# Kernel optimization log

Measured on AMD Instinct MI355X. Metric: run time of the kernel, lower is better.

The kernel has to match this reference:

```python
import jax, jax.numpy as jnp
import numpy as np
import math

B, S, D, H = 16, 1024, 1024, 16
HD = D // H                      # 64 head dim
MLP_H = int(int(D * 4.0) * 2 / 3)  # 2730 SwiGLU hidden
EPS = 1e-6


def _rmsnorm(h, w):
    # fp32 RMSNorm over last dim
    v = jnp.mean(h * h, axis=-1, keepdims=True)
    return w * (h * jax.lax.rsqrt(v + EPS))


def _rope(x):
    # x: [B, H, S, HD]; standard rotary, half-split convention
    hd = x.shape[-1]
    pos = jnp.arange(x.shape[-2], dtype=jnp.float32)
    inv = 1.0 / (10000.0 ** (jnp.arange(0, hd, 2, dtype=jnp.float32) / hd))
    fr = pos[:, None] * inv[None, :]          # [S, HD/2]
    cos, sin = jnp.cos(fr), jnp.sin(fr)
    x1, x2 = jnp.split(x, 2, axis=-1)
    return jnp.concatenate([x1 * cos - x2 * sin, x1 * sin + x2 * cos], axis=-1)


def setup_inputs() -> dict:
    key = jax.random.key(0)
    ks = jax.random.split(key, 16)
    sc = 0.02
    return {
        "x": jax.random.normal(ks[0], (B, S, D), jnp.float32),
        "c": jax.random.normal(ks[1], (B, D), jnp.float32),
        "w_qkv": jax.random.normal(ks[2], (D, 3 * D), jnp.float32) * sc,
        "b_qkv": jnp.zeros((3 * D,), jnp.float32),
        "w_proj": jax.random.normal(ks[3], (D, D), jnp.float32) * sc,
        "b_proj": jnp.zeros((D,), jnp.float32),
        "w12": jax.random.normal(ks[4], (D, 2 * MLP_H), jnp.float32) * sc,
        "b12": jnp.zeros((2 * MLP_H,), jnp.float32),
        "w3": jax.random.normal(ks[5], (MLP_H, D), jnp.float32) * sc,
        "b3": jnp.zeros((D,), jnp.float32),
        "w_ada": jax.random.normal(ks[6], (D, 6 * D), jnp.float32) * sc,
        "b_ada": jnp.zeros((6 * D,), jnp.float32),
        "norm1_w": jnp.ones((D,), jnp.float32),
        "norm2_w": jnp.ones((D,), jnp.float32),
        "qn_w": jnp.ones((HD,), jnp.float32),
        "kn_w": jnp.ones((HD,), jnp.float32),
    }


def _forward(x, c, w_qkv, b_qkv, w_proj, b_proj, w12, b12, w3, b3,
             w_ada, b_ada, norm1_w, norm2_w, qn_w, kn_w):
    # adaLN modulation params
    ada = jax.nn.silu(c) @ w_ada + b_ada               # [B, 6D]
    sh_a, sc_a, g_a, sh_m, sc_m, g_m = jnp.split(ada, 6, axis=-1)

    def modulate(h, shift, scale):
        return h * (1.0 + scale[:, None, :]) + shift[:, None, :]

    # --- attention branch ---
    h = modulate(_rmsnorm(x, norm1_w), sh_a, sc_a)     # [B, S, D]
    qkv = (h @ w_qkv + b_qkv).reshape(B, S, 3, H, HD)
    qkv = jnp.transpose(qkv, (2, 0, 3, 1, 4))          # [3, B, H, S, HD]
    q, k, v = qkv[0], qkv[1], qkv[2]
    q = _rope(_rmsnorm(q, qn_w))
    k = _rope(_rmsnorm(k, kn_w))
    scores = jnp.einsum('bhqd,bhkd->bhqk', q, k) / math.sqrt(HD)
    attn = jax.nn.softmax(scores, axis=-1)
    o = jnp.einsum('bhqk,bhkd->bhqd', attn, v)         # [B, H, S, HD]
    o = jnp.transpose(o, (0, 2, 1, 3)).reshape(B, S, D)
    o = o @ w_proj + b_proj
    x = x + g_a[:, None, :] * o

    # --- SwiGLU MLP branch ---
    h = modulate(_rmsnorm(x, norm2_w), sh_m, sc_m)
    x12 = h @ w12 + b12
    x1, x2 = jnp.split(x12, 2, axis=-1)
    mlp = (jax.nn.silu(x1) * x2) @ w3 + b3
    return x + g_m[:, None, :] * mlp


def reference(x, c, w_qkv, b_qkv, w_proj, b_proj, w12, b12, w3, b3,
              w_ada, b_ada, norm1_w, norm2_w, qn_w, kn_w):
    return _forward(x, c, w_qkv, b_qkv, w_proj, b_proj, w12, b12, w3, b3,
                    w_ada, b_ada, norm1_w, norm2_w, qn_w, kn_w)
```

## Files before the change

### kernel.cpp

```cpp
#include <hip/hip_runtime.h>
#include <hip/hip_bf16.h>
#include <math.h>

namespace {

constexpr int Bb = 16;
constexpr int Ss = 1024;
constexpr int Dd = 1024;
constexpr int Hh = 16;
constexpr int HD = 64;
constexpr int MLPH = 2730;
constexpr int MLPH_PAD = 2752;
constexpr int ADA_LD = 6144;
constexpr int NR = Bb * Ss;

typedef __attribute__((ext_vector_type(8))) short bf16x8;
typedef __attribute__((ext_vector_type(4))) float f32x4;
typedef __hip_bfloat16 bf16;
typedef unsigned int u32;

__device__ __forceinline__ float bf2f(bf16 v){ return __bfloat162float(v); }
__device__ __forceinline__ bf16 f2bf(float v){ return __float2bfloat16(v); }
__device__ __forceinline__ short f2bfs(float v){ bf16 t = __float2bfloat16(v); return __builtin_bit_cast(short, t); }

__device__ __forceinline__ f32x4 mfma16(bf16x8 a, bf16x8 b, f32x4 c){
  return __builtin_amdgcn_mfma_f32_16x16x32_bf16(a, b, c, 0, 0, 0);
}

__device__ __forceinline__ void gload16(const void* g, void* l){
  __builtin_amdgcn_global_load_lds(
      (const __attribute__((address_space(1))) u32*)g,
      (__attribute__((address_space(3))) u32*)l, 16, 0, 0);
}


__global__ void k_silu(const float* __restrict__ c, float* __restrict__ out, int n){
  int i = blockIdx.x*256 + threadIdx.x;
  if(i < n){ float v = c[i]; out[i] = v / (1.f + __expf(-v)); }
}

__global__ __launch_bounds__(256) void k_ada(const float* __restrict__ sc,
    const float* __restrict__ w, const float* __restrict__ bias, float* __restrict__ ada){
  __shared__ float red[4][Bb][64];
  int tid = threadIdx.x;
  int jj = tid & 63, ks = tid >> 6;
  int j = blockIdx.x*64 + jj;
  float acc[Bb];
  #pragma unroll
  for(int b=0;b<Bb;++b) acc[b] = 0.f;
  for(int k=ks*256; k<ks*256+256; ++k){
    float wv = w[(size_t)k*ADA_LD + j];
    #pragma unroll
    for(int b=0;b<Bb;++b) acc[b] += sc[b*Dd + k] * wv;
  }
  #pragma unroll
  for(int b=0;b<Bb;++b) red[ks][b][jj] = acc[b];
  __syncthreads();
  #pragma unroll
  for(int rep=0;rep<4;++rep){
    int idx = rep*256 + tid;
    int b = idx >> 6, j2 = idx & 63;
    float s = red[0][b][j2]+red[1][b][j2]+red[2][b][j2]+red[3][b][j2];
    ada[(size_t)b*ADA_LD + blockIdx.x*64 + j2] = s + bias[blockIdx.x*64 + j2];
  }
}

__global__ void k_rope_tab(float2* __restrict__ tab){
  int i = blockIdx.x*256 + threadIdx.x;
  int s = i >> 5, f = i & 31;
  float inv = powf(10000.f, -((float)(2*f)) / 64.f);
  float fr = (float)s * inv;
  float sv, cv;
  sincosf(fr, &sv, &cv);
  tab[i] = make_float2(cv, sv);
}

__global__ void k_transpose(const float* __restrict__ in, bf16* __restrict__ out,
                            int R, int C, int Rpad){
  __shared__ short tile[32][33];
  int tx = threadIdx.x & 31, ty = threadIdx.x >> 5;
  int tr0 = blockIdx.x*32, tc0 = blockIdx.y*32;
  #pragma unroll
  for(int i=0;i<4;++i){
    int r = tr0 + ty + i*8, cc = tc0 + tx;
    short v = 0;
    if(r < R && cc < C) v = f2bfs(in[(size_t)r*C + cc]);
    tile[ty+i*8][tx] = v;
  }
  __syncthreads();
  #pragma unroll
  for(int i=0;i<4;++i){
    int oc = tc0 + ty + i*8;
    int orow = tr0 + tx;
    if(oc < C && orow < Rpad)
      out[(size_t)oc*Rpad + orow] = __builtin_bit_cast(bf16, tile[tx][ty+i*8]);
  }
}

__global__ __launch_bounds__(256) void k_norm_mod(const float* __restrict__ x,
    const float* __restrict__ w, const float* __restrict__ shift, const float* __restrict__ scale,
    bf16* __restrict__ out){
  int r = blockIdx.x;
  int b = r >> 10;
  int t = threadIdx.x;
  const float* xr = x + (size_t)r*Dd;
  float v[4]; float ss = 0.f;
  #pragma unroll
  for(int i=0;i<4;++i){
    float f = xr[t*4+i];
    v[i] = f; ss += f*f;
  }
  #pragma unroll
  for(int m=1;m<64;m<<=1) ss += __shfl_xor(ss, m);
  __shared__ float red[4];
  if((t & 63) == 0) red[t>>6] = ss;
  __syncthreads();
  float tot = red[0]+red[1]+red[2]+red[3];
  float rms = rsqrtf(tot * (1.f/Dd) + 1e-6f);
  #pragma unroll
  for(int i=0;i<4;++i){
    int ccol = t*4+i;
    float h = v[i]*rms*w[ccol];
    float scv = scale[(size_t)b*ADA_LD + ccol];
    float shv = shift[(size_t)b*ADA_LD + ccol];
    out[(size_t)r*Dd + ccol] = f2bf(h*(1.f+scv) + shv);
  }
}

__global__ __launch_bounds__(256) void k_qknorm(bf16* __restrict__ qkv,
    const float* __restrict__ qw, const float* __restrict__ kw,
    const float2* __restrict__ tab){
  int bs = blockIdx.x;
  int s = bs & (Ss-1);
  int tid = threadIdx.x;
  int wv = tid >> 6, lane = tid & 63;
  int isK = wv >> 1;
  int chunk = (wv & 1)*64 + lane;
  int c = chunk & 7;
  int h = chunk >> 3;
  int dih = c*8;
  bf16* p = qkv + (size_t)bs*3072 + isK*Dd + h*HD + dih;
  bf16x8 v = *(const bf16x8*)p;
  float x[8]; float ss = 0.f;
  #pragma unroll
  for(int i=0;i<8;++i){ x[i] = bf2f(__builtin_bit_cast(bf16,(short)v[i])); ss += x[i]*x[i]; }
  ss += __shfl_xor(ss,1); ss += __shfl_xor(ss,2); ss += __shfl_xor(ss,4);
  float rms = rsqrtf(ss*(1.f/HD) + 1e-6f);
  const float* wn = isK ? kw : qw;
  float xn[8];
  #pragma unroll
  for(int i=0;i<8;++i) xn[i] = x[i]*rms*wn[dih+i];
  u32 pk[4], pq[4];
  #pragma unroll
  for(int i=0;i<4;++i)
    pk[i] = (u32)(unsigned short)f2bfs(xn[2*i]) |
            ((u32)(unsigned short)f2bfs(xn[2*i+1]) << 16);
  #pragma unroll
  for(int i=0;i<4;++i) pq[i] = __shfl_xor((int)pk[i], 4);
  float px[8];
  #pragma unroll
  for(int i=0;i<4;++i){
    px[2*i]   = bf2f(__builtin_bit_cast(bf16,(short)(pq[i] & 0xffff)));
    px[2*i+1] = bf2f(__builtin_bit_cast(bf16,(short)(pq[i] >> 16)));
  }
  const float2* tb = tab + s*32 + (c & 3)*8;
  float qs = isK ? 1.f : 0.18033688f;
  bf16x8 o;
  #pragma unroll
  for(int i=0;i<8;++i){
    float2 cs = tb[i];
    float r = (c < 4) ? (xn[i]*cs.x - px[i]*cs.y) : (px[i]*cs.y + xn[i]*cs.x);
    o[i] = f2bfs(r*qs);
  }
  *(bf16x8*)p = o;
}

template<int MODE>
__global__ __launch_bounds__(256, 2) void k_gemm(
    const bf16* __restrict__ A, int lda,
    const bf16* __restrict__ BT, long long b2off, int ldb,
    const float* __restrict__ bias1, const float* __restrict__ bias2,
    int K,
    const float* __restrict__ res, const float* __restrict__ gate,
    void* __restrict__ outp, int ldo)
{
  constexpr int BN  = (MODE==3) ? 64 : 128;
  constexpr int NFR = (MODE==3) ? 2  : 4;
  alignas(16) __shared__ short As[2][128*32];
  alignas(16) __shared__ short Bs[2][BN*32];
  alignas(16) __shared__ short Bs2[(MODE==3)?2:1][(MODE==3)?BN*32:8];

  int tid = threadIdx.x;
  int lane = tid & 63, wid = tid >> 6;
  int wm = wid >> 1, wn = wid & 1;
  int l15 = lane & 15, l4 = lane >> 4;
  int brow = blockIdx.x * 128;
  int bcol = blockIdx.y * BN;

  int r0 = tid >> 2, s0 = tid & 3;
  int r1 = r0 + 64;
  int k80 = s0 ^ ((r0 >> 1) & 3);
  int k81 = s0 ^ ((r1 >> 1) & 3);

  const bf16* a0 = A  + (size_t)(brow+r0)*lda + k80*8;
  const bf16* a1 = A  + (size_t)(brow+r1)*lda + k81*8;
  const bf16* b0 = BT + (size_t)(bcol+r0)*ldb + k80*8;
  const bf16* b1 = BT + (size_t)(bcol+r1)*ldb + k81*8;

  f32x4 zero4 = {0.f,0.f,0.f,0.f};
  f32x4 acc[4][NFR], acc2[4][NFR];
  #pragma unroll
  for(int m=0;m<4;++m)
    #pragma unroll
    for(int n=0;n<NFR;++n){ acc[m][n]=zero4; acc2[m][n]=zero4; }

  auto STAGE = [&](int kt, int buf){
    int ko = kt << 5;
    gload16(a0 + ko, &As[buf][tid*8]);
    gload16(a1 + ko, &As[buf][(tid+256)*8]);
    gload16(b0 + ko, &Bs[buf][tid*8]);
    if constexpr (MODE!=3) gload16(b1 + ko, &Bs[buf][(tid+256)*8]);
    if constexpr (MODE==3) gload16(b0 + b2off + ko, &Bs2[buf][tid*8]);
  };

  const int nk = K >> 5;
  STAGE(0, 0);
  __syncthreads();

  int cur = 0;
  for(int kt=0; kt<nk; ++kt){
    if(kt+1 < nk) STAGE(kt+1, cur^1);

    bf16x8 af[4], bfr[NFR], bfr2[NFR];
    #pragma unroll
    for(int m=0;m<4;++m){
      int rr = wm*64 + m*16 + l15;
      int sl = l4 ^ ((rr >> 1) & 3);
      af[m] = *(const bf16x8*)&As[cur][rr*32 + sl*8];
    }
    #pragma unroll
    for(int n=0;n<NFR;++n){
      int rr = wn*(16*NFR) + n*16 + l15;
      int sl = l4 ^ ((rr >> 1) & 3);
      bfr[n] = *(const bf16x8*)&Bs[cur][rr*32 + sl*8];
      if constexpr (MODE==3)
        bfr2[n] = *(const bf16x8*)&Bs2[cur][rr*32 + sl*8];
    }
    #pragma unroll
    for(int m=0;m<4;++m){
      #pragma unroll
      for(int n=0;n<NFR;++n){
        acc[m][n] = mfma16(af[m], bfr[n], acc[m][n]);
        if constexpr (MODE==3) acc2[m][n] = mfma16(af[m], bfr2[n], acc2[m][n]);
      }
    }
    __syncthreads();
    cur ^= 1;
  }

  #pragma unroll
  for(int m=0;m<4;++m){
    #pragma unroll
    for(int n=0;n<NFR;++n){
      #pragma unroll
      for(int j=0;j<4;++j){
        int r  = brow + wm*64 + m*16 + l4*4 + j;
        int cc = bcol + wn*(16*NFR) + n*16 + l15;
        float v = acc[m][n][j];
        if constexpr (MODE==0){
          v += bias1[cc];
          ((bf16*)outp)[(size_t)r*ldo + cc] = f2bf(v);
        } else if constexpr (MODE==1){
          v += bias1[cc];
          int b = r >> 10;
          float xr = res[(size_t)r*Dd + cc];
          ((float*)outp)[(size_t)r*ldo + cc] = xr + gate[(size_t)b*ADA_LD + cc]*v;
        } else {
          float o = 0.f;
          if(cc < MLPH){
            float v1 = v + bias1[cc];
            float v2 = acc2[m][n][j] + bias2[cc];
            o = (v1/(1.f+__expf(-v1)))*v2;
          }
          ((bf16*)outp)[(size_t)r*ldo + cc] = f2bf(o);
        }
      }
    }
  }
}

__global__ __launch_bounds__(256) void k_attn(const bf16* __restrict__ qkv, bf16* __restrict__ obuf){
  alignas(16) __shared__ short Ks[64*64];
  alignas(16) __shared__ short VTs[64*64];
  alignas(16) __shared__ short Ps[128*64];

  int flatb = blockIdx.x;
  int low3 = flatb & 7;
  int rest = flatb >> 3;
  int qb   = rest & 7;
  int bh   = ((rest >> 3) << 3) | low3;
  int b = bh >> 4, h = bh & 15;

  int tid = threadIdx.x;
  int lane = tid & 63, w = tid >> 6;
  int l15 = lane & 15, l4 = lane >> 4;

  const bf16* base = qkv + (size_t)b*Ss*3072 + h*HD;

  bf16x8 aq[2][2];
  #pragma unroll
  for(int hi=0;hi<2;++hi)
    #pragma unroll
    for(int hf=0;hf<2;++hf)
      aq[hi][hf] = *(const bf16x8*)(base +
          (size_t)(qb*128 + w*32 + hi*16 + l15)*3072 + hf*32 + l4*8);

  int r0 = tid >> 3, c0 = tid & 7;
  int khcol = (c0 ^ (r0 & 7)) * 8;
  bf16x8 kreg[2], vreg[2];
  #pragma unroll
  for(int ch=0; ch<2; ++ch){
    int rr = r0 + ch*32;
    kreg[ch] = *(const bf16x8*)(base + Dd   + (size_t)rr*3072 + khcol);
    vreg[ch] = *(const bf16x8*)(base + 2*Dd + (size_t)rr*3072 + c0*8);
  }

  f32x4 zero4 = {0.f,0.f,0.f,0.f};
  f32x4 acc_o[2][4];
  float mrow[2], lrow[2];
  #pragma unroll
  for(int hi=0;hi<2;++hi){
    mrow[hi] = -1e30f; lrow[hi] = 0.f;
    #pragma unroll
    for(int an=0;an<4;++an) acc_o[hi][an] = zero4;
  }

  const float THR = 11.54f;

  for(int kb=0; kb<Ss/64; ++kb){
    if(kb) __syncthreads();
    #pragma unroll
    for(int ch=0; ch<2; ++ch){
      *(bf16x8*)&Ks[(tid + ch*256)*8] = kreg[ch];
      int vr = r0 + ch*32;
      #pragma unroll
      for(int i=0;i<8;++i){
        int g = i ^ c0;
        VTs[(c0*8 + i)*64 + (vr ^ (g<<3))] = vreg[ch][i];
      }
    }
    if(kb+1 < Ss/64){
      #pragma unroll
      for(int ch=0; ch<2; ++ch){
        int rr = (kb+1)*64 + r0 + ch*32;
        kreg[ch] = *(const bf16x8*)(base + Dd   + (size_t)rr*3072 + khcol);
        vreg[ch] = *(const bf16x8*)(base + 2*Dd + (size_t)rr*3072 + c0*8);
      }
    }
    __syncthreads();

    #pragma unroll
    for(int hi=0; hi<2; ++hi){
      f32x4 sacc[4];
      #pragma unroll
      for(int an=0;an<4;++an) sacc[an]=zero4;
      __builtin_amdgcn_s_setprio(1);
      #pragma unroll
      for(int an=0;an<4;++an){
        int R = an*16 + l15;
        bf16x8 bk0 = *(const bf16x8*)&Ks[R*64 + ((l4     ^ (R&7)))*8];
        bf16x8 bk1 = *(const bf16x8*)&Ks[R*64 + (((4|l4) ^ (R&7)))*8];
        sacc[an] = mfma16(bk0, aq[hi][0], sacc[an]);
        sacc[an] = mfma16(bk1, aq[hi][1], sacc[an]);
      }
      __builtin_amdgcn_s_setprio(0);

      float mx = -1e30f;
      #pragma unroll
      for(int an=0;an<4;++an)
        #pragma unroll
        for(int j=0;j<4;++j) mx = fmaxf(mx, sacc[an][j]);
      mx = fmaxf(mx, __shfl_xor(mx, 16));
      mx = fmaxf(mx, __shfl_xor(mx, 32));
      bool grow = mx > mrow[hi] + THR;
      if(__any(grow)){
        float mnew = fmaxf(mrow[hi], mx);
        float corr = exp2f(mrow[hi] - mnew);
        mrow[hi] = mnew;
        lrow[hi] *= corr;
        float cj[4];
        #pragma unroll
        for(int j=0;j<4;++j) cj[j] = __shfl(corr, l4*4 + j);
        #pragma unroll
        for(int an=0;an<4;++an)
          #pragma unroll
          for(int j=0;j<4;++j) acc_o[hi][an][j] *= cj[j];
      }
      float psum = 0.f;
      #pragma unroll
      for(int an=0;an<4;++an)
        #pragma unroll
        for(int j=0;j<4;++j){
          float pv = exp2f(sacc[an][j] - mrow[hi]);
          sacc[an][j] = pv; psum += pv;
        }
      psum += __shfl_xor(psum, 16);
      psum += __shfl_xor(psum, 32);
      lrow[hi] += psum;

      int prow = w*32 + hi*16 + l15;
      int pg = (l15 & 7) << 3;
      #pragma unroll
      for(int an=0;an<4;++an)
        #pragma unroll
        for(int j=0;j<4;++j)
          Ps[prow*64 + ((an*16 + l4*4 + j) ^ pg)] = f2bfs(sacc[an][j]);
      bf16x8 pa0 = *(const bf16x8*)&Ps[prow*64 + ((l4*8)      ^ pg)];
      bf16x8 pa1 = *(const bf16x8*)&Ps[prow*64 + ((32 + l4*8) ^ pg)];
      __builtin_amdgcn_s_setprio(1);
      #pragma unroll
      for(int an2=0;an2<4;++an2){
        int dR = an2*16 + l15;
        int g = ((dR & 7) ^ ((dR >> 3) & 7)) << 3;
        bf16x8 bv0 = *(const bf16x8*)&VTs[dR*64 + ((l4*8)      ^ g)];
        bf16x8 bv1 = *(const bf16x8*)&VTs[dR*64 + ((32 + l4*8) ^ g)];
        acc_o[hi][an2] = mfma16(pa0, bv0, acc_o[hi][an2]);
        acc_o[hi][an2] = mfma16(pa1, bv1, acc_o[hi][an2]);
      }
      __builtin_amdgcn_s_setprio(0);
    }
  }
  #pragma unroll
  for(int hi=0;hi<2;++hi){
    float lr[4];
    #pragma unroll
    for(int j=0;j<4;++j) lr[j] = __shfl(lrow[hi], l4*4 + j);
    #pragma unroll
    for(int an2=0;an2<4;++an2)
      #pragma unroll
      for(int j=0;j<4;++j){
        int r = qb*128 + w*32 + hi*16 + l4*4 + j;
        float ov = acc_o[hi][an2][j] / lr[j];
        obuf[((size_t)b*Ss + r)*Dd + h*HD + an2*16 + l15] = f2bf(ov);
      }
  }
}

}

extern "C" void kernel_launch(void* const* d_in, const int* in_sizes, int n_in,
                              void* d_out, int out_size, void* d_ws, size_t ws_size,
                              hipStream_t stream){
  const float* x      = (const float*)d_in[0];
  const float* c      = (const float*)d_in[1];
  const float* w_qkv  = (const float*)d_in[2];
  const float* b_qkv  = (const float*)d_in[3];
  const float* w_proj = (const float*)d_in[4];
  const float* b_proj = (const float*)d_in[5];
  const float* w12    = (const float*)d_in[6];
  const float* b12    = (const float*)d_in[7];
  const float* w3     = (const float*)d_in[8];
  const float* b3     = (const float*)d_in[9];
  const float* w_ada  = (const float*)d_in[10];
  const float* b_ada  = (const float*)d_in[11];
  const float* n1w    = (const float*)d_in[12];
  const float* n2w    = (const float*)d_in[13];
  const float* qnw    = (const float*)d_in[14];
  const float* knw    = (const float*)d_in[15];
  float* out = (float*)d_out;
  (void)in_sizes; (void)n_in; (void)out_size;

  constexpr size_t WS_NEED = 227254272ull;
  if (ws_size < WS_NEED) return;

  char* ws = (char*)d_ws;
  float*  silu_c = (float*)(ws + 0);
  float*  ada    = (float*)(ws + 65536);
  float2* ropet  = (float2*)(ws + 458752);
  bf16*   wqkvT  = (bf16*)(ws + 720896);
  bf16*   wprojT = (bf16*)(ws + 7012352);
  bf16*   w12T   = (bf16*)(ws + 9109504);
  bf16*   w3T    = (bf16*)(ws + 20291584);
  bf16*   hbuf   = (bf16*)(ws + 25927680);
  bf16*   qkvb   = (bf16*)(ws + 59482112);
  float*  xmid   = (float*)(ws + 160145408);
  bf16*   obuf   = hbuf;
  bf16*   h2     = hbuf;
  bf16*   mlpmid = qkvb;

  k_silu<<<64,256,0,stream>>>(c, silu_c, Bb*Dd);
  k_rope_tab<<<128,256,0,stream>>>(ropet);
  k_ada<<<96,256,0,stream>>>(silu_c, w_ada, b_ada, ada);
  k_transpose<<<dim3(32,96),256,0,stream>>>(w_qkv, wqkvT, 1024, 3072, 1024);
  k_transpose<<<dim3(32,32),256,0,stream>>>(w_proj, wprojT, 1024, 1024, 1024);
  k_transpose<<<dim3(32,171),256,0,stream>>>(w12, w12T, 1024, 5460, 1024);
  k_transpose<<<dim3(86,32),256,0,stream>>>(w3, w3T, 2730, 1024, 2752);

  k_norm_mod<<<NR,256,0,stream>>>(x, n1w, ada + 0, ada + 1024, hbuf);
  k_gemm<0><<<dim3(128,24),256,0,stream>>>(hbuf,1024, wqkvT,0,1024,
      b_qkv,nullptr, 1024, nullptr,nullptr, qkvb,3072);
  k_qknorm<<<NR,256,0,stream>>>(qkvb, qnw, knw, ropet);
  k_attn<<<2048,256,0,stream>>>(qkvb, obuf);
  k_gemm<1><<<dim3(128,8),256,0,stream>>>(obuf,1024, wprojT,0,1024,
      b_proj,nullptr, 1024, x, ada + 2048, xmid,1024);

  k_norm_mod<<<NR,256,0,stream>>>(xmid, n2w, ada + 3072, ada + 4096, h2);
  k_gemm<3><<<dim3(128,43),256,0,stream>>>(h2,1024, w12T,(long long)MLPH*1024,1024,
      b12, b12 + MLPH, 1024, nullptr,nullptr, mlpmid, MLPH_PAD);
  k_gemm<1><<<dim3(128,8),256,0,stream>>>(mlpmid,MLPH_PAD, w3T,0,MLPH_PAD,
      b3,nullptr, MLPH_PAD, xmid, ada + 5120, out,1024);
}
```

Measured before the change: 937.7 us.

## Add 256x256 eight-wave pipelined GEMM for QKV, proj and down GEMMs

Adds a new GEMM kernel with 512 threads and 256x256 output tiles, K-steps of 64, and separate A and B half-tile LDS buffers. Loads for the next steps are interleaved with four MFMA phases, using explicit barriers, waitcnt and setprio. It is used for the QKV, attention-projection and MLP down-projection GEMMs. The SwiGLU up-projection keeps the old kernel as a specialised k_gemm3. The goal is more data reuse per tile and better overlap of global loads with MFMA. The cost is about 128KB of LDS per block, which likely allows only one block per CU, and hand-written wait counts that could be fragile.

```diff
diff --git a/kernel.cpp b/kernel.cpp
--- a/kernel.cpp
+++ b/kernel.cpp
@@ -175,27 +175,135 @@
   *(bf16x8*)p = o;
 }
 
+#define LDA8(M,KH) (*(const bf16x8*)&Ah[((M)*16 + l15)*64 + ((((KH)*4 + l4) ^ l7))*8])
+#define PHASE8(M0, STAGE_STMT, GATE_STMT) do{ \
+  bf16x8 a0k0 = LDA8(M0,0), a0k1 = LDA8(M0,1), a1k0 = LDA8(M0+1,0), a1k1 = LDA8(M0+1,1); \
+  STAGE_STMT; \
+  __builtin_amdgcn_s_barrier(); \
+  asm volatile("s_waitcnt lgkmcnt(0)" ::: "memory"); \
+  __builtin_amdgcn_sched_barrier(0); \
+  __builtin_amdgcn_s_setprio(1); \
+  acc[M0][0]=mfma16(a0k0,bfrag[0][0],acc[M0][0]); acc[M0][0]=mfma16(a0k1,bfrag[0][1],acc[M0][0]); \
+  acc[M0][1]=mfma16(a0k0,bfrag[1][0],acc[M0][1]); acc[M0][1]=mfma16(a0k1,bfrag[1][1],acc[M0][1]); \
+  acc[M0][2]=mfma16(a0k0,bfrag[2][0],acc[M0][2]); acc[M0][2]=mfma16(a0k1,bfrag[2][1],acc[M0][2]); \
+  acc[M0][3]=mfma16(a0k0,bfrag[3][0],acc[M0][3]); acc[M0][3]=mfma16(a0k1,bfrag[3][1],acc[M0][3]); \
+  acc[M0+1][0]=mfma16(a1k0,bfrag[0][0],acc[M0+1][0]); acc[M0+1][0]=mfma16(a1k1,bfrag[0][1],acc[M0+1][0]); \
+  acc[M0+1][1]=mfma16(a1k0,bfrag[1][0],acc[M0+1][1]); acc[M0+1][1]=mfma16(a1k1,bfrag[1][1],acc[M0+1][1]); \
+  acc[M0+1][2]=mfma16(a1k0,bfrag[2][0],acc[M0+1][2]); acc[M0+1][2]=mfma16(a1k1,bfrag[2][1],acc[M0+1][2]); \
+  acc[M0+1][3]=mfma16(a1k0,bfrag[3][0],acc[M0+1][3]); acc[M0+1][3]=mfma16(a1k1,bfrag[3][1],acc[M0+1][3]); \
+  __builtin_amdgcn_s_setprio(0); \
+  GATE_STMT; \
+  __builtin_amdgcn_s_barrier(); }while(0)
+
 template<int MODE>
-__global__ __launch_bounds__(256, 2) void k_gemm(
+__global__ __launch_bounds__(512, 2) void k_gemm8(
+    const bf16* __restrict__ A, int lda,
+    const bf16* __restrict__ BT, int ldb,
+    const float* __restrict__ bias1, int K,
+    const float* __restrict__ res, const float* __restrict__ gate,
+    void* __restrict__ outp, int ldo)
+{
+  alignas(16) __shared__ short AH[2][2][128*64];
+  alignas(16) __shared__ short BH[2][2][128*64];
+
+  const int tid = threadIdx.x;
+  const int lane = tid & 63, wid = tid >> 6;
+  const int wm = wid >> 2, wn = wid & 3;
+  const int l15 = lane & 15, l4 = lane >> 4;
+  const int l7 = l15 & 7;
+  const int brow = blockIdx.x * 256;
+  const int bcol = blockIdx.y * 256;
+
+  const int sr0 = tid >> 3;
+  const int sr1 = sr0 + 64;
+  const int sc  = ((tid & 7) ^ (sr0 & 7)) * 8;
+
+  const bf16* Abase = A  + (size_t)brow*lda;
+  const bf16* Bbase = BT + (size_t)bcol*ldb;
+
+  auto stageA = [&](int t, int h){
+    int d = t & 1;
+    const bf16* g = Abase + (size_t)(h*128)*lda + t*64;
+    gload16(g + (size_t)sr0*lda + sc, &AH[d][h][tid*8]);
+    gload16(g + (size_t)sr1*lda + sc, &AH[d][h][(tid+512)*8]);
+  };
+  auto stageB = [&](int t, int h){
+    int d = t & 1;
+    const bf16* g = Bbase + (size_t)(h*128)*ldb + t*64;
+    gload16(g + (size_t)sr0*ldb + sc, &BH[d][h][tid*8]);
+    gload16(g + (size_t)sr1*ldb + sc, &BH[d][h][(tid+512)*8]);
+  };
+
+  f32x4 acc[8][4];
+  f32x4 zero4 = {0.f,0.f,0.f,0.f};
+  #pragma unroll
+  for(int m=0;m<8;++m)
+    #pragma unroll
+    for(int n=0;n<4;++n) acc[m][n] = zero4;
+
+  const int NT = K >> 6;
+  stageA(0,0); stageA(0,1); stageB(0,0); stageB(0,1);
+  stageB(1,0); stageB(1,1);
+  asm volatile("s_waitcnt vmcnt(4)" ::: "memory");
+  __builtin_amdgcn_sched_barrier(0);
+  __builtin_amdgcn_s_barrier();
+
+  const int bhsel = wn >> 1, brB = (wn & 1)*64;
+  bf16x8 bfrag[4][2];
+
+  for(int t=0; t<NT; ++t){
+    const int d = t & 1;
+    const short* Ah = AH[d][wm];
+    const short* Bh = BH[d][bhsel];
+    #pragma unroll
+    for(int n=0;n<4;++n){
+      int r = brB + n*16 + l15;
+      bfrag[n][0] = *(const bf16x8*)&Bh[r*64 + ((l4     ^ l7))*8];
+      bfrag[n][1] = *(const bf16x8*)&Bh[r*64 + (((4|l4) ^ l7))*8];
+    }
+    PHASE8(0, if(t+1 < NT) stageA(t+1,0), );
+    PHASE8(2, if(t+1 < NT) stageA(t+1,1), );
+    PHASE8(4, if(t+2 < NT) stageB(t+2,0), );
+    PHASE8(6, if(t+2 < NT) stageB(t+2,1),
+           asm volatile("s_waitcnt vmcnt(4)" ::: "memory");
+           __builtin_amdgcn_sched_barrier(0) );
+  }
+
+  #pragma unroll
+  for(int m=0;m<8;++m)
+    #pragma unroll
+    for(int n=0;n<4;++n)
+      #pragma unroll
+      for(int j=0;j<4;++j){
+        int r  = brow + wm*128 + m*16 + l4*4 + j;
+        int cc = bcol + wn*64  + n*16 + l15;
+        float v = acc[m][n][j] + bias1[cc];
+        if constexpr (MODE==0){
+          ((bf16*)outp)[(size_t)r*ldo + cc] = f2bf(v);
+        } else {
+          int b = r >> 10;
+          ((float*)outp)[(size_t)r*ldo + cc] =
+              res[(size_t)r*Dd + cc] + gate[(size_t)b*ADA_LD + cc]*v;
+        }
+      }
+}
+
+__global__ __launch_bounds__(256, 2) void k_gemm3(
     const bf16* __restrict__ A, int lda,
     const bf16* __restrict__ BT, long long b2off, int ldb,
     const float* __restrict__ bias1, const float* __restrict__ bias2,
-    int K,
-    const float* __restrict__ res, const float* __restrict__ gate,
-    void* __restrict__ outp, int ldo)
+    int K, bf16* __restrict__ outp, int ldo)
 {
-  constexpr int BN  = (MODE==3) ? 64 : 128;
-  constexpr int NFR = (MODE==3) ? 2  : 4;
   alignas(16) __shared__ short As[2][128*32];
-  alignas(16) __shared__ short Bs[2][BN*32];
-  alignas(16) __shared__ short Bs2[(MODE==3)?2:1][(MODE==3)?BN*32:8];
+  alignas(16) __shared__ short Bs[2][64*32];
+  alignas(16) __shared__ short Bs2[2][64*32];
 
   int tid = threadIdx.x;
   int lane = tid & 63, wid = tid >> 6;
   int wm = wid >> 1, wn = wid & 1;
   int l15 = lane & 15, l4 = lane >> 4;
   int brow = blockIdx.x * 128;
-  int bcol = blockIdx.y * BN;
+  int bcol = blockIdx.y * 64;
 
   int r0 = tid >> 2, s0 = tid & 3;
   int r1 = r0 + 64;
@@ -205,22 +313,20 @@
   const bf16* a0 = A  + (size_t)(brow+r0)*lda + k80*8;
   const bf16* a1 = A  + (size_t)(brow+r1)*lda + k81*8;
   const bf16* b0 = BT + (size_t)(bcol+r0)*ldb + k80*8;
-  const bf16* b1 = BT + (size_t)(bcol+r1)*ldb + k81*8;
 
   f32x4 zero4 = {0.f,0.f,0.f,0.f};
-  f32x4 acc[4][NFR], acc2[4][NFR];
+  f32x4 acc[4][2], acc2[4][2];
   #pragma unroll
   for(int m=0;m<4;++m)
     #pragma unroll
-    for(int n=0;n<NFR;++n){ acc[m][n]=zero4; acc2[m][n]=zero4; }
+    for(int n=0;n<2;++n){ acc[m][n]=zero4; acc2[m][n]=zero4; }
 
   auto STAGE = [&](int kt, int buf){
     int ko = kt << 5;
     gload16(a0 + ko, &As[buf][tid*8]);
     gload16(a1 + ko, &As[buf][(tid+256)*8]);
     gload16(b0 + ko, &Bs[buf][tid*8]);
-    if constexpr (MODE!=3) gload16(b1 + ko, &Bs[buf][(tid+256)*8]);
-    if constexpr (MODE==3) gload16(b0 + b2off + ko, &Bs2[buf][tid*8]);
+    gload16(b0 + b2off + ko, &Bs2[buf][tid*8]);
   };
 
   const int nk = K >> 5;
@@ -230,8 +336,7 @@
   int cur = 0;
   for(int kt=0; kt<nk; ++kt){
     if(kt+1 < nk) STAGE(kt+1, cur^1);
-
-    bf16x8 af[4], bfr[NFR], bfr2[NFR];
+    bf16x8 af[4], bfr[2], bfr2[2];
     #pragma unroll
     for(int m=0;m<4;++m){
       int rr = wm*64 + m*16 + l15;
@@ -239,54 +344,39 @@
       af[m] = *(const bf16x8*)&As[cur][rr*32 + sl*8];
     }
     #pragma unroll
-    for(int n=0;n<NFR;++n){
-      int rr = wn*(16*NFR) + n*16 + l15;
+    for(int n=0;n<2;++n){
+      int rr = wn*32 + n*16 + l15;
       int sl = l4 ^ ((rr >> 1) & 3);
-      bfr[n] = *(const bf16x8*)&Bs[cur][rr*32 + sl*8];
-      if constexpr (MODE==3)
-        bfr2[n] = *(const bf16x8*)&Bs2[cur][rr*32 + sl*8];
+      bfr[n]  = *(const bf16x8*)&Bs[cur][rr*32 + sl*8];
+      bfr2[n] = *(const bf16x8*)&Bs2[cur][rr*32 + sl*8];
     }
     #pragma unroll
-    for(int m=0;m<4;++m){
-      #pragma unroll
-      for(int n=0;n<NFR;++n){
-        acc[m][n] = mfma16(af[m], bfr[n], acc[m][n]);
-        if constexpr (MODE==3) acc2[m][n] = mfma16(af[m], bfr2[n], acc2[m][n]);
-      }
-    }
+    for(int m=0;m<4;++m)
+      #pragma unroll
+      for(int n=0;n<2;++n){
+        acc[m][n]  = mfma16(af[m], bfr[n],  acc[m][n]);
+        acc2[m][n] = mfma16(af[m], bfr2[n], acc2[m][n]);
+      }
     __syncthreads();
     cur ^= 1;
   }
 
   #pragma unroll
-  for(int m=0;m<4;++m){
-    #pragma unroll
-    for(int n=0;n<NFR;++n){
+  for(int m=0;m<4;++m)
+    #pragma unroll
+    for(int n=0;n<2;++n)
       #pragma unroll
       for(int j=0;j<4;++j){
         int r  = brow + wm*64 + m*16 + l4*4 + j;
-        int cc = bcol + wn*(16*NFR) + n*16 + l15;
-        float v = acc[m][n][j];
-        if constexpr (MODE==0){
-          v += bias1[cc];
-          ((bf16*)outp)[(size_t)r*ldo + cc] = f2bf(v);
-        } else if constexpr (MODE==1){
-          v += bias1[cc];
-          int b = r >> 10;
-          float xr = res[(size_t)r*Dd + cc];
-          ((float*)outp)[(size_t)r*ldo + cc] = xr + gate[(size_t)b*ADA_LD + cc]*v;
-        } else {
-          float o = 0.f;
-          if(cc < MLPH){
-            float v1 = v + bias1[cc];
-            float v2 = acc2[m][n][j] + bias2[cc];
-            o = (v1/(1.f+__expf(-v1)))*v2;
-          }
-          ((bf16*)outp)[(size_t)r*ldo + cc] = f2bf(o);
+        int cc = bcol + wn*32 + n*16 + l15;
+        float o = 0.f;
+        if(cc < MLPH){
+          float v1 = acc[m][n][j] + bias1[cc];
+          float v2 = acc2[m][n][j] + bias2[cc];
+          o = (v1/(1.f+__expf(-v1)))*v2;
         }
-      }
-    }
-  }
+        outp[(size_t)r*ldo + cc] = f2bf(o);
+      }
 }
 
 __global__ __launch_bounds__(256) void k_attn(const bf16* __restrict__ qkv, bf16* __restrict__ obuf){
@@ -497,16 +587,16 @@
   k_transpose<<<dim3(86,32),256,0,stream>>>(w3, w3T, 2730, 1024, 2752);
 
   k_norm_mod<<<NR,256,0,stream>>>(x, n1w, ada + 0, ada + 1024, hbuf);
-  k_gemm<0><<<dim3(128,24),256,0,stream>>>(hbuf,1024, wqkvT,0,1024,
-      b_qkv,nullptr, 1024, nullptr,nullptr, qkvb,3072);
+  k_gemm8<0><<<dim3(64,12),512,0,stream>>>(hbuf,1024, wqkvT,1024,
+      b_qkv, 1024, nullptr,nullptr, qkvb,3072);
   k_qknorm<<<NR,256,0,stream>>>(qkvb, qnw, knw, ropet);
   k_attn<<<2048,256,0,stream>>>(qkvb, obuf);
-  k_gemm<1><<<dim3(128,8),256,0,stream>>>(obuf,1024, wprojT,0,1024,
-      b_proj,nullptr, 1024, x, ada + 2048, xmid,1024);
+  k_gemm8<1><<<dim3(64,4),512,0,stream>>>(obuf,1024, wprojT,1024,
+      b_proj, 1024, x, ada + 2048, xmid,1024);
 
   k_norm_mod<<<NR,256,0,stream>>>(xmid, n2w, ada + 3072, ada + 4096, h2);
-  k_gemm<3><<<dim3(128,43),256,0,stream>>>(h2,1024, w12T,(long long)MLPH*1024,1024,
-      b12, b12 + MLPH, 1024, nullptr,nullptr, mlpmid, MLPH_PAD);
-  k_gemm<1><<<dim3(128,8),256,0,stream>>>(mlpmid,MLPH_PAD, w3T,0,MLPH_PAD,
-      b3,nullptr, MLPH_PAD, xmid, ada + 5120, out,1024);
-}
+  k_gemm3<<<dim3(128,43),256,0,stream>>>(h2,1024, w12T,(long long)MLPH*1024,1024,
+      b12, b12 + MLPH, 1024, mlpmid, MLPH_PAD);
+  k_gemm8<1><<<dim3(64,4),512,0,stream>>>(mlpmid,MLPH_PAD, w3T,MLPH_PAD,
+      b3, MLPH_PAD, xmid, ada + 5120, out,1024);
+}
```

New measurement: 891.5 us. 4.9% less time.
